# Performance work log

Hardware: AMD Instinct MI355X
Metric: run time of the kernel (lower is better)

Reference implementation:

```python
import jax, jax.numpy as jnp
import numpy as np

B, S, H, L = 128, 2048, 512, 11

def setup_inputs() -> dict:
    key = jax.random.key(0)
    k1, k2, k3, k4 = jax.random.split(key, 4)
    return {
        "find_contri": 1,
        "code_output": jax.random.normal(k1, (B, S, H), dtype=jnp.float32),
        "lengths": jax.random.randint(k2, (B,), 1, S + 1),  # ragged lengths in [1, S]
        "contri": jax.random.uniform(k3, (B, S, 2), dtype=jnp.float32),
        "fc_w": jax.random.normal(k4, (L, H), dtype=jnp.float32) * 0.05,
    }

def reference(find_contri, code_output, lengths, contri, fc_w):
    b, s, h = code_output.shape
    # Faithful to torch .view (reshape, not transpose): [B,S,H] -> [B,H,S]
    x = code_output.reshape(b, h, s)
    # Ragged adaptive max-pool to size 1 with indices: mask positions >= length
    valid = jnp.arange(s)[None, :] < lengths[:, None]            # [B,S]
    xm = jnp.where(valid[:, None, :], x, -jnp.inf)               # [B,H,S]
    code_pool = jnp.max(xm, axis=2)                              # [B,H]
    code_indices = jnp.argmax(xm, axis=2)                        # [B,H], in [0,len)
    attn = code_pool @ fc_w.T                                    # [B,11], no bias
    if find_contri:
        # con[lab,i] = relu(pool[i]*fc_w[lab]) + 1e-4, normalized to sum 100.
        # Original mutates one `contri` tensor across all labs and appends the
        # same reference 11 times; the final state is the sum over labs.
        p10 = code_pool[:10]                                     # only first 10 samples
        con = jax.nn.relu(p10[:, None, :] * fc_w[None, :, :]) + 1e-4   # [10,11,H]
        con = con / jnp.sum(con, axis=2, keepdims=True) * 100.0
        total = jnp.sum(con, axis=1)                             # [10,H]
        # indexed scatter-add into the new third channel
        scat = jax.vmap(lambda idx, c: jnp.zeros((s,), total.dtype).at[idx].add(c))(
            code_indices[:10], total)                            # [10,S]
        ch2 = jnp.zeros((b, s), contri.dtype).at[:10].set(scat)  # [B,S]
        contri_out = jnp.concatenate([contri, ch2[..., None]], axis=2)  # [B,S,3]
        return attn, contri_out
    return attn
```

## Files before the change

### kernel.cpp

```cpp
#include <hip/hip_runtime.h>
#include <math.h>

#define BB 128
#define SS 2048
#define HH 512
#define LL 11

typedef float vf4 __attribute__((ext_vector_type(4)));

#define COPYBLK 944

__global__ __launch_bounds__(256) void rowmax_kernel(
    const float* __restrict__ x,
    const int* __restrict__ lengths,
    const float* __restrict__ contri,
    float* __restrict__ pool,
    int* __restrict__ idx_out,
    float* __restrict__ out2) {
  if (blockIdx.x < COPYBLK) {
    int i = blockIdx.x * 256 + threadIdx.x;
    int t = 10 * SS + i;
    out2[t * 3 + 0] = contri[t * 2 + 0];
    out2[t * 3 + 1] = contri[t * 2 + 1];
    out2[t * 3 + 2] = 0.f;
    return;
  }

  int wave = (blockIdx.x - COPYBLK) * 4 + (threadIdx.x >> 6);
  int lane = threadIdx.x & 63;
  int b = wave >> 9;
  int len = lengths[b];
  const vf4* row = (const vf4*)(x + (size_t)wave * SS);

  int nj = (len + 255) >> 8;

  float best = -INFINITY;
  int bidx = 0;
  vf4 v = row[lane];
  for (int j = 0; j < nj; ++j) {
    vf4 nxt = v;
    if (j + 1 < nj)
      nxt = row[(j + 1) * 64 + lane];
    int si = (j * 64 + lane) * 4;
    float a;
    a = (si + 0 < len) ? v.x : -INFINITY;
    if (a > best) { best = a; bidx = si + 0; }
    a = (si + 1 < len) ? v.y : -INFINITY;
    if (a > best) { best = a; bidx = si + 1; }
    a = (si + 2 < len) ? v.z : -INFINITY;
    if (a > best) { best = a; bidx = si + 2; }
    a = (si + 3 < len) ? v.w : -INFINITY;
    if (a > best) { best = a; bidx = si + 3; }
    v = nxt;
  }

#pragma unroll
  for (int off = 32; off > 0; off >>= 1) {
    float ov = __shfl_down(best, off);
    int oi = __shfl_down(bidx, off);
    if (ov > best || (ov == best && oi < bidx)) { best = ov; bidx = oi; }
  }
  if (lane == 0) {
    pool[wave] = best;
    idx_out[wave] = bidx;
  }
}

__global__ __launch_bounds__(256) void epilogue_kernel(
    const float* __restrict__ pool,
    const int* __restrict__ idx_in,
    const float* __restrict__ fcw,
    const float* __restrict__ contri,
    float* __restrict__ attn_out,
    float* __restrict__ out2) {
  int tid = threadIdx.x;
  int wv = tid >> 6;
  int lane = tid & 63;

  if (blockIdx.x < 10) {
    int b = blockIdx.x;
    __shared__ float sp[HH];
    __shared__ float sden[LL];
    __shared__ float sch[SS];

    for (int h = tid; h < HH; h += 256) sp[h] = pool[b * HH + h];
    for (int s = tid; s < SS; s += 256) sch[s] = 0.f;
    __syncthreads();

    for (int l = wv; l < LL; l += 4) {
      float s = 0.f;
#pragma unroll
      for (int k = 0; k < HH / 64; ++k) {
        int h = k * 64 + lane;
        s += fmaxf(sp[h] * fcw[l * HH + h], 0.f);
      }
#pragma unroll
      for (int off = 32; off > 0; off >>= 1) s += __shfl_down(s, off);
      if (lane == 0) sden[l] = 100.f / (s + (float)HH * 1e-4f);
    }
    __syncthreads();

    for (int hh = tid; hh < HH; hh += 256) {
      float p = sp[hh];
      float tot = 0.f;
#pragma unroll
      for (int l = 0; l < LL; ++l)
        tot += (fmaxf(p * fcw[l * HH + hh], 0.f) + 1e-4f) * sden[l];
      atomicAdd(&sch[idx_in[b * HH + hh]], tot);
    }
    __syncthreads();

    for (int s = tid; s < SS; s += 256) {
      int t = b * SS + s;
      out2[t * 3 + 0] = contri[t * 2 + 0];
      out2[t * 3 + 1] = contri[t * 2 + 1];
      out2[t * 3 + 2] = sch[s];
    }
  } else {
    int b = blockIdx.x - 10;
    const float* p = pool + b * HH;
    for (int l = wv; l < LL; l += 4) {
      const float* w = fcw + l * HH;
      float s = 0.f;
#pragma unroll
      for (int k = 0; k < HH / 64; ++k) s += p[k * 64 + lane] * w[k * 64 + lane];
#pragma unroll
      for (int off = 32; off > 0; off >>= 1) s += __shfl_down(s, off);
      if (lane == 0) attn_out[b * LL + l] = s;
    }
  }
}

extern "C" void kernel_launch(void* const* d_in, const int* in_sizes, int n_in,
                              void* d_out, int out_size, void* d_ws, size_t ws_size,
                              hipStream_t stream) {
  const float* code_output = (const float*)d_in[1];
  const int* lengths = (const int*)d_in[2];
  const float* contri = (const float*)d_in[3];
  const float* fcw = (const float*)d_in[4];

  float* out = (float*)d_out;
  float* out2 = out + BB * LL;

  float* ws = (float*)d_ws;
  float* pool = ws;
  int* idx = (int*)(ws + BB * HH);

  int row_blocks = (BB * HH) / 4;
  rowmax_kernel<<<COPYBLK + row_blocks, 256, 0, stream>>>(
      code_output, lengths, contri, pool, idx, out2);

  epilogue_kernel<<<10 + BB, 256, 0, stream>>>(pool, idx, fcw, contri, out, out2);
}
```

Before: 645.8 us.

## Issue all row loads upfront and vectorize contri copy blocks

```diff
diff --git a/kernel.cpp b/kernel.cpp
--- a/kernel.cpp
+++ b/kernel.cpp
@@ -8,7 +8,7 @@
 
 typedef float vf4 __attribute__((ext_vector_type(4)));
 
-#define COPYBLK 944
+#define COPYBLK 236
 
 __global__ __launch_bounds__(256) void rowmax_kernel(
     const float* __restrict__ x,
@@ -18,11 +18,16 @@
     int* __restrict__ idx_out,
     float* __restrict__ out2) {
   if (blockIdx.x < COPYBLK) {
-    int i = blockIdx.x * 256 + threadIdx.x;
-    int t = 10 * SS + i;
-    out2[t * 3 + 0] = contri[t * 2 + 0];
-    out2[t * 3 + 1] = contri[t * 2 + 1];
-    out2[t * 3 + 2] = 0.f;
+    int i4 = blockIdx.x * 256 + threadIdx.x;
+    int t = 10 * SS + i4 * 4;
+    vf4 c0 = *(const vf4*)(contri + (size_t)t * 2);
+    vf4 c1 = *(const vf4*)(contri + (size_t)t * 2 + 4);
+    vf4 o0, o1, o2;
+    o0.x = c0.x; o0.y = c0.y; o0.z = 0.f; o0.w = c0.z;
+    o1.x = c0.w; o1.y = 0.f;  o1.z = c1.x; o1.w = c1.y;
+    o2.x = 0.f;  o2.y = c1.z; o2.z = c1.w; o2.w = 0.f;
+    vf4* dst = (vf4*)(out2 + (size_t)t * 3);
+    dst[0] = o0; dst[1] = o1; dst[2] = o2;
     return;
   }
 
@@ -31,28 +36,42 @@
   int b = wave >> 9;
   int len = lengths[b];
   const vf4* row = (const vf4*)(x + (size_t)wave * SS);
+  int nj = (len + 255) >> 8;
 
-  int nj = (len + 255) >> 8;
+  vf4 v0, v1, v2, v3, v4, v5, v6, v7;
+  v0 = row[lane];
+  if (nj > 1) v1 = row[1 * 64 + lane];
+  if (nj > 2) v2 = row[2 * 64 + lane];
+  if (nj > 3) v3 = row[3 * 64 + lane];
+  if (nj > 4) v4 = row[4 * 64 + lane];
+  if (nj > 5) v5 = row[5 * 64 + lane];
+  if (nj > 6) v6 = row[6 * 64 + lane];
+  if (nj > 7) v7 = row[7 * 64 + lane];
 
   float best = -INFINITY;
   int bidx = 0;
-  vf4 v = row[lane];
-  for (int j = 0; j < nj; ++j) {
-    vf4 nxt = v;
-    if (j + 1 < nj)
-      nxt = row[(j + 1) * 64 + lane];
-    int si = (j * 64 + lane) * 4;
-    float a;
-    a = (si + 0 < len) ? v.x : -INFINITY;
-    if (a > best) { best = a; bidx = si + 0; }
-    a = (si + 1 < len) ? v.y : -INFINITY;
-    if (a > best) { best = a; bidx = si + 1; }
-    a = (si + 2 < len) ? v.z : -INFINITY;
-    if (a > best) { best = a; bidx = si + 2; }
-    a = (si + 3 < len) ? v.w : -INFINITY;
-    if (a > best) { best = a; bidx = si + 3; }
-    v = nxt;
+#define PROC(vv, J)                                              \
+  {                                                              \
+    int si = ((J) * 64 + lane) * 4;                              \
+    float a;                                                     \
+    a = (si + 0 < len) ? (vv).x : -INFINITY;                     \
+    if (a > best) { best = a; bidx = si + 0; }                   \
+    a = (si + 1 < len) ? (vv).y : -INFINITY;                     \
+    if (a > best) { best = a; bidx = si + 1; }                   \
+    a = (si + 2 < len) ? (vv).z : -INFINITY;                     \
+    if (a > best) { best = a; bidx = si + 2; }                   \
+    a = (si + 3 < len) ? (vv).w : -INFINITY;                     \
+    if (a > best) { best = a; bidx = si + 3; }                   \
   }
+  PROC(v0, 0);
+  if (nj > 1) PROC(v1, 1);
+  if (nj > 2) PROC(v2, 2);
+  if (nj > 3) PROC(v3, 3);
+  if (nj > 4) PROC(v4, 4);
+  if (nj > 5) PROC(v5, 5);
+  if (nj > 6) PROC(v6, 6);
+  if (nj > 7) PROC(v7, 7);
+#undef PROC
 
 #pragma unroll
   for (int off = 32; off > 0; off >>= 1) {
```

New measurement: 645.7 us. Within noise of the previous version (-0.0%).
